# Performance work log

Hardware: AMD Instinct MI355X
Metric: run time of the kernel (lower is better)

Reference implementation:

```python
import jax, jax.numpy as jnp
import numpy as np

EPS = 1e-8
LAMBDA_SOFTMAX = 9.0
LAMBDA_LSE = 6.0
MARGIN = 0.2


def setup_inputs() -> dict:
    key = jax.random.key(0)
    k1, k2, k3 = jax.random.split(key, 3)
    B, R, W, D = 128, 36, 64, 1024
    im = jax.random.normal(k1, (B, R, D), dtype=jnp.float32)
    s = jax.random.normal(k2, (B, W, D), dtype=jnp.float32)
    s_l = jax.random.randint(k3, (B,), 8, W + 1, dtype=jnp.int32)
    return {"im": im, "s": s, "s_l": s_l}


def _xattn_scores_t2i(im, s, s_l):
    # im: [B, R, D] images; s: [B, W, D] captions; s_l: [B] caption lengths
    B, W = s.shape[0], s.shape[1]
    wmask = (jnp.arange(W)[None, :] < s_l[:, None]).astype(im.dtype)  # [B, W]

    def per_caption(args):
        cap, wm = args  # cap: [W, D], wm: [W]
        # raw attention: context=images, query=caption words -> [B, R, W]
        attn = jnp.einsum('ird,wd->irw', im, cap)
        # clipped_l2norm: leakyrelu(0.1) then l2norm over word dim; padded words zeroed
        attn = jax.nn.leaky_relu(attn, 0.1) * wm
        attn = attn / (jnp.sqrt(jnp.sum(attn * attn, axis=2, keepdims=True)) + EPS)
        # transpose to [B, W, R], softmax over regions with smoothing
        attn = jax.nn.softmax(jnp.swapaxes(attn, 1, 2) * LAMBDA_SOFTMAX, axis=2)
        # weighted image context per word: [B, W, D]
        wei = jnp.einsum('iwr,ird->iwd', attn, im)
        # cosine similarity between caption words and weighted context
        num = jnp.einsum('iwd,wd->iw', wei, cap)
        n_cap = jnp.sqrt(jnp.sum(cap * cap, axis=-1))      # [W]
        n_wei = jnp.sqrt(jnp.sum(wei * wei, axis=-1))      # [B, W]
        row = num / jnp.maximum(n_cap[None, :] * n_wei, EPS)
        # LogSumExp aggregation over valid words -> [B]
        return jnp.log(jnp.sum(jnp.exp(LAMBDA_LSE * row) * wm[None, :], axis=1)) / LAMBDA_LSE

    cols = jax.lax.map(per_caption, (s, wmask))  # [B_cap, B_img]
    return cols.T  # scores[i, j]: image i vs caption j


def reference(im, s, s_l):
    scores = _xattn_scores_t2i(im, s, s_l)  # [B, B]
    B = scores.shape[0]
    diag = jnp.diagonal(scores)[:, None]  # [B, 1]
    cost_s = jnp.clip(MARGIN + scores - diag, 0.0)       # caption retrieval
    cost_im = jnp.clip(MARGIN + scores - diag.T, 0.0)    # image retrieval
    off = 1.0 - jnp.eye(B, dtype=scores.dtype)
    cost_s = cost_s * off
    cost_im = cost_im * off
    # max_violation=True: hardest negatives
    cost_s = jnp.max(cost_s, axis=1)
    cost_im = jnp.max(cost_im, axis=0)
    return jnp.sum(cost_s) + jnp.sum(cost_im)
```

## Files before the change

### kernel.cpp

```cpp
#include <hip/hip_runtime.h>
#include <hip/hip_bf16.h>
#include <math.h>
#include <stdint.h>

#define NB 128
#define NR 36
#define NW 64
#define ND 1024
#define MT 48
#define EPSF 1e-8f
#define LAM_SM 9.0f
#define LAM_LSE 6.0f
#define MARGINF 0.2f

typedef _Float16 f16;
typedef f16 f16x4 __attribute__((ext_vector_type(4)));
typedef f16 f16x8 __attribute__((ext_vector_type(8)));
typedef float f32x4 __attribute__((ext_vector_type(4)));
typedef int i32x4 __attribute__((ext_vector_type(4)));
typedef int i32x8 __attribute__((ext_vector_type(8)));

__device__ __forceinline__ uint32_t pk_fp8x4(float4 v) {
    uint32_t w = 0;
    w = __builtin_amdgcn_cvt_pk_fp8_f32(v.x, v.y, w, false);
    w = __builtin_amdgcn_cvt_pk_fp8_f32(v.z, v.w, w, true);
    return w;
}


__global__ __launch_bounds__(256) void prep_kernel(
    const float* __restrict__ im, const float* __restrict__ s,
    uint8_t* __restrict__ im8, uint8_t* __restrict__ s8, float* __restrict__ ncap,
    f16* __restrict__ Mg16) {
    __shared__ __align__(16) char Gs[8192];
    const int b = blockIdx.x, y = blockIdx.y, t = threadIdx.x;

    if (y < 14) {
        const int lr = t >> 5, g = t & 31;
        const int row = y * 8 + lr;
        if (row < MT) {
            const int mi = row >> 4, l16 = row & 15;
            uint32_t* dstd = (uint32_t*)im8;
            if (row < NR) {
                const float4* src = (const float4*)(im + ((size_t)b * NR + row) * ND);
                #pragma unroll
                for (int e = 0; e < 8; ++e) {
                    int di = g + e * 32;
                    int kc = di >> 5, q = (di >> 3) & 3, bw = di & 7;
                    size_t dst = ((size_t)(b * 8 + kc) * 3 + mi) * 512
                                 + (q * 16 + l16) * 8 + bw;
                    dstd[dst] = pk_fp8x4(src[di]);
                }
            } else {
                #pragma unroll
                for (int e = 0; e < 8; ++e) {
                    int di = g + e * 32;
                    int kc = di >> 5, q = (di >> 3) & 3, bw = di & 7;
                    size_t dst = ((size_t)(b * 8 + kc) * 3 + mi) * 512
                                 + (q * 16 + l16) * 8 + bw;
                    dstd[dst] = 0u;
                }
            }
        } else {
            const int w = row - MT;
            const int nt = w >> 4, l16 = w & 15;
            const float4* src = (const float4*)(s + ((size_t)b * NW + w) * ND);
            uint32_t* dstd = (uint32_t*)s8;
            float ss = 0.f;
            #pragma unroll
            for (int e = 0; e < 8; ++e) {
                int di = g + e * 32;
                int kc = di >> 5, q = (di >> 3) & 3, bw = di & 7;
                float4 v = src[di];
                size_t dst = ((size_t)(b * 8 + kc) * 4 + nt) * 512
                             + (q * 16 + l16) * 8 + bw;
                dstd[dst] = pk_fp8x4(v);
                ss += v.x * v.x + v.y * v.y + v.z * v.z + v.w * v.w;
            }
            #pragma unroll
            for (int off = 1; off < 32; off <<= 1) ss += __shfl_xor(ss, off, 32);
            if (g == 0) ncap[b * NW + w] = sqrtf(ss);
        }
        return;
    }

    const int wave = t >> 6, lane = t & 63;
    const int quad = lane >> 4, l16 = lane & 15;
    const int nt = wave;
    f32x4 acc[3];
    acc[0] = (f32x4){0.f, 0.f, 0.f, 0.f};
    acc[1] = (f32x4){0.f, 0.f, 0.f, 0.f};
    acc[2] = (f32x4){0.f, 0.f, 0.f, 0.f};
    const float* imb = im + (size_t)b * NR * ND;

    for (int kk = 0; kk < ND; kk += 64) {
        for (int cidx = t; cidx < 512; cidx += 256) {
            int row = cidx >> 3, c = cidx & 7;
            f16x8 hv;
            if (row < NR) {
                const float4* sp = (const float4*)(imb + (size_t)row * ND + kk + c * 8);
                float4 v0 = sp[0], v1 = sp[1];
                hv = (f16x8){(f16)v0.x, (f16)v0.y, (f16)v0.z, (f16)v0.w,
                             (f16)v1.x, (f16)v1.y, (f16)v1.z, (f16)v1.w};
            } else {
                hv = (f16x8){(f16)0.f, (f16)0.f, (f16)0.f, (f16)0.f,
                             (f16)0.f, (f16)0.f, (f16)0.f, (f16)0.f};
            }
            *(f16x8*)(Gs + row * 128 + ((c ^ (row & 7)) * 16)) = hv;
        }
        __syncthreads();
        #pragma unroll
        for (int ks = 0; ks < 2; ++ks) {
            int brow = nt * 16 + l16;
            f16x8 bf = *(const f16x8*)(Gs + brow * 128 + (((ks * 4 + quad) ^ (brow & 7)) * 16));
            #pragma unroll
            for (int mt = 0; mt < 3; ++mt) {
                int arow = mt * 16 + l16;
                f16x8 af = *(const f16x8*)(Gs + arow * 128 + (((ks * 4 + quad) ^ (arow & 7)) * 16));
                acc[mt] = __builtin_amdgcn_mfma_f32_16x16x32_f16(af, bf, acc[mt], 0, 0, 0);
            }
        }
        __syncthreads();
    }
    f16* Mb = Mg16 + (size_t)b * (MT * NW);
    #pragma unroll
    for (int mt = 0; mt < 3; ++mt) {
        #pragma unroll
        for (int r = 0; r < 4; ++r) {
            int row = mt * 16 + quad * 4 + r;
            Mb[row * NW + nt * 16 + l16] = (f16)acc[mt][r];
        }
    }
}

__global__ __launch_bounds__(256) void fused_pair_kernel(
    const uint8_t* __restrict__ im8, const uint8_t* __restrict__ s8,
    const int* __restrict__ s_l, const f16* __restrict__ Mg16,
    const float* __restrict__ ncap, float* __restrict__ scores) {
    __shared__ __align__(16) char lds[32768];
    const int t = threadIdx.x;
    const int wave = t >> 6, lane = t & 63;
    const int quad = lane >> 4, l16 = lane & 15;
    const int wi = wave >> 1, wj = wave & 1;

    const int lin = blockIdx.x;
    const int gx = lin & 63, gy = lin >> 6;
    const int i = gy * 2 + wi;
    const int j = gx * 2 + wj;
    const int L = s_l[j];

    f32x4 acc[3][4];
    #pragma unroll
    for (int mi = 0; mi < 3; ++mi)
        #pragma unroll
        for (int nt = 0; nt < 4; ++nt)
            acc[mi][nt] = (f32x4){0.f, 0.f, 0.f, 0.f};

    const uint8_t* Afrag = im8 + (size_t)i * (8 * 3 * 2048) + lane * 32;
    const uint8_t* Bfrag = s8 + (size_t)j * (8 * 4 * 2048) + lane * 32;

    #pragma unroll 1
    for (int kc = 0; kc < 8; ++kc) {
        const uint8_t* Ak = Afrag + (size_t)kc * (3 * 2048);
        const uint8_t* Bk = Bfrag + (size_t)kc * (4 * 2048);
        i32x8 bf[4];
        #pragma unroll
        for (int nt = 0; nt < 4; ++nt)
            bf[nt] = *(const i32x8*)(Bk + nt * 2048);
        #pragma unroll
        for (int mi = 0; mi < 3; ++mi) {
            i32x8 af = *(const i32x8*)(Ak + mi * 2048);
            #pragma unroll
            for (int nt = 0; nt < 4; ++nt)
                acc[mi][nt] = __builtin_amdgcn_mfma_scale_f32_16x16x128_f8f6f4(
                    af, bf[nt], acc[mi][nt], 0, 0, 0, 0x7F, 0, 0x7F);
        }
    }

    char* waveE = lds + wave * 8192;
    {
        int col = lane;
        f16x8 z = {(f16)0.f,(f16)0.f,(f16)0.f,(f16)0.f,(f16)0.f,(f16)0.f,(f16)0.f,(f16)0.f};
        *(f16x8*)(waveE + col * 128 + ((6 ^ (col & 7)) * 16)) = z;
        *(f16x8*)(waveE + col * 128 + ((7 ^ (col & 7)) * 16)) = z;
    }

    float rn[3][4];
    #pragma unroll
    for (int mi = 0; mi < 3; ++mi) {
        #pragma unroll
        for (int r = 0; r < 4; ++r) {
            int row = mi * 16 + quad * 4 + r;
            float ss = 0.f;
            #pragma unroll
            for (int nt = 0; nt < 4; ++nt) {
                int col = nt * 16 + l16;
                float v = acc[mi][nt][r];
                float lv = v > 0.f ? v : 0.1f * v;
                if (col < L) ss += lv * lv;
            }
            ss += __shfl_xor(ss, 1, 64);
            ss += __shfl_xor(ss, 2, 64);
            ss += __shfl_xor(ss, 4, 64);
            ss += __shfl_xor(ss, 8, 64);
            rn[mi][r] = (row < NR) ? 1.0f / (sqrtf(ss) + EPSF) : 0.f;
        }
    }
    float cs[4] = {0.f, 0.f, 0.f, 0.f}, nu[4] = {0.f, 0.f, 0.f, 0.f};
    #pragma unroll
    for (int mi = 0; mi < 3; ++mi) {
        #pragma unroll
        for (int nt = 0; nt < 4; ++nt) {
            int col = nt * 16 + l16;
            f16x4 ew;
            #pragma unroll
            for (int r = 0; r < 4; ++r) {
                float v = acc[mi][nt][r];
                float lv = v > 0.f ? v : 0.1f * v;
                float e = __expf(LAM_SM * ((col < L) ? lv * rn[mi][r] : 0.f));
                ew[r] = (f16)e;
                if (mi * 16 + quad * 4 + r < NR) { cs[nt] += e; nu[nt] += e * v; }
            }
            int c = mi * 2 + (quad >> 1);
            *(f16x4*)(waveE + col * 128 + ((c ^ (col & 7)) * 16) + (quad & 1) * 8) = ew;
        }
    }
    #pragma unroll
    for (int nt = 0; nt < 4; ++nt) {
        cs[nt] += __shfl_xor(cs[nt], 16, 64); cs[nt] += __shfl_xor(cs[nt], 32, 64);
        nu[nt] += __shfl_xor(nu[nt], 16, 64); nu[nt] += __shfl_xor(nu[nt], 32, 64);
    }

    const f16* Mi = Mg16 + (size_t)i * (MT * NW);
    float qf[4] = {0.f, 0.f, 0.f, 0.f};
    #pragma unroll
    for (int mi = 0; mi < 3; ++mi) {
        f32x4 y[4];
        #pragma unroll
        for (int nt = 0; nt < 4; ++nt) y[nt] = (f32x4){0.f, 0.f, 0.f, 0.f};
        #pragma unroll
        for (int ks = 0; ks < 2; ++ks) {
            f16x8 aq = *(const f16x8*)(Mi + (mi * 16 + l16) * NW + ks * 32 + quad * 8);
            #pragma unroll
            for (int nt = 0; nt < 4; ++nt) {
                int col = nt * 16 + l16;
                int pch = (ks * 4 + quad) ^ (col & 7);
                f16x8 bq = *(const f16x8*)(waveE + col * 128 + pch * 16);
                y[nt] = __builtin_amdgcn_mfma_f32_16x16x32_f16(aq, bq, y[nt], 0, 0, 0);
            }
        }
        int row0 = mi * 16 + quad * 4;
        int c = row0 >> 3, sub = (row0 >> 2) & 1;
        #pragma unroll
        for (int nt = 0; nt < 4; ++nt) {
            int col = nt * 16 + l16;
            f16x4 ev = *(const f16x4*)(waveE + col * 128 + ((c ^ (col & 7)) * 16) + sub * 8);
            #pragma unroll
            for (int r = 0; r < 4; ++r) qf[nt] += y[nt][r] * (float)ev[r];
        }
    }
    #pragma unroll
    for (int nt = 0; nt < 4; ++nt) {
        qf[nt] += __shfl_xor(qf[nt], 16, 64); qf[nt] += __shfl_xor(qf[nt], 32, 64);
    }
    float lse = 0.f;
    #pragma unroll
    for (int nt = 0; nt < 4; ++nt) {
        int col = nt * 16 + l16;
        float num  = nu[nt] / cs[nt];
        float nwei = sqrtf(fmaxf(qf[nt], 0.f)) / cs[nt];
        float nc   = ncap[j * NW + col];
        float rowv = num / fmaxf(nc * nwei, EPSF);
        lse += (col < L) ? __expf(LAM_LSE * rowv) : 0.f;
    }
    lse += __shfl_xor(lse, 1, 64);
    lse += __shfl_xor(lse, 2, 64);
    lse += __shfl_xor(lse, 4, 64);
    lse += __shfl_xor(lse, 8, 64);
    if (lane == 0) scores[i * NB + j] = __logf(lse) / LAM_LSE;
}

__global__ __launch_bounds__(256) void loss_kernel(const float* __restrict__ S,
                                                   float* __restrict__ out) {
    __shared__ __align__(16) float Sl[NB * NB];
    __shared__ float part[NB];
    __shared__ float wsum[2];
    int t = threadIdx.x;
    for (int c = t; c < (NB * NB) / 4; c += 256)
        ((float4*)Sl)[c] = ((const float4*)S)[c];
    __syncthreads();
    if (t < NB) {
        float dii = Sl[t * NB + t];
        float rmax = 0.f, cmax = 0.f;
        for (int k = 0; k < NB; ++k) {
            if (k != t) {
                float vs = MARGINF + Sl[t * NB + k] - dii;
                rmax = fmaxf(rmax, fmaxf(vs, 0.f));
                float vi = MARGINF + Sl[k * NB + t] - dii;
                cmax = fmaxf(cmax, fmaxf(vi, 0.f));
            }
        }
        part[t] = rmax + cmax;
    }
    __syncthreads();
    if (t < NB) {
        float v = part[t];
        #pragma unroll
        for (int off = 1; off < 64; off <<= 1) v += __shfl_xor(v, off, 64);
        if ((t & 63) == 0) wsum[t >> 6] = v;
    }
    __syncthreads();
    if (t == 0) out[0] = wsum[0] + wsum[1];
}

extern "C" void kernel_launch(void* const* d_in, const int* in_sizes, int n_in,
                              void* d_out, int out_size, void* d_ws, size_t ws_size,
                              hipStream_t stream) {
    const float* im  = (const float*)d_in[0];
    const float* s   = (const float*)d_in[1];
    const int*   s_l = (const int*)d_in[2];

    float*   scores = (float*)d_ws;
    float*   ncap   = scores + NB * NB;
    f16*     Mg16   = (f16*)(ncap + NB * NW);
    uint8_t* im8    = (uint8_t*)(Mg16 + (size_t)NB * MT * NW);
    uint8_t* s8     = im8 + (size_t)NB * MT * ND;

    dim3 pgrid(NB, 15);
    prep_kernel<<<pgrid, 256, 0, stream>>>(im, s, im8, s8, ncap, Mg16);
    fused_pair_kernel<<<4096, 256, 0, stream>>>(im8, s8, s_l, Mg16, ncap, scores);
    loss_kernel<<<1, 256, 0, stream>>>(scores, (float*)d_out);
}
```

Measured before the change: 212.0 us.

## Double-buffer FP8 fragment loads in pair kernel and skew loss-kernel row reads

Replaces the rolled k-loop in the fused pair kernel with a fully unrolled, register double-buffered sequence. The global fragment loads for chunk k+1 are issued before the 12 MFMAs of chunk k, so memory latency overlaps with matrix compute. The loss kernel now walks each row starting at a per-thread rotated column, which spreads LDS accesses across banks instead of every thread hitting the same bank. The cost is roughly double the registers held for fragments, which may lower occupancy.

```diff
diff --git a/kernel.cpp b/kernel.cpp
--- a/kernel.cpp
+++ b/kernel.cpp
@@ -133,6 +133,38 @@
     }
 }
 
+
+__device__ __forceinline__ void load_frags(
+    const uint8_t* __restrict__ Af, const uint8_t* __restrict__ Bf, int kc,
+    i32x8& a0, i32x8& a1, i32x8& a2,
+    i32x8& b0, i32x8& b1, i32x8& b2, i32x8& b3) {
+    const uint8_t* Ak = Af + kc * (3 * 2048);
+    const uint8_t* Bk = Bf + kc * (4 * 2048);
+    a0 = *(const i32x8*)(Ak);
+    a1 = *(const i32x8*)(Ak + 2048);
+    a2 = *(const i32x8*)(Ak + 4096);
+    b0 = *(const i32x8*)(Bk);
+    b1 = *(const i32x8*)(Bk + 2048);
+    b2 = *(const i32x8*)(Bk + 4096);
+    b3 = *(const i32x8*)(Bk + 6144);
+}
+
+#define MFMA12(A0, A1, A2, B0, B1, B2, B3)                                        \
+    do {                                                                          \
+        acc[0][0] = __builtin_amdgcn_mfma_scale_f32_16x16x128_f8f6f4(A0, B0, acc[0][0], 0, 0, 0, 0x7F, 0, 0x7F); \
+        acc[0][1] = __builtin_amdgcn_mfma_scale_f32_16x16x128_f8f6f4(A0, B1, acc[0][1], 0, 0, 0, 0x7F, 0, 0x7F); \
+        acc[0][2] = __builtin_amdgcn_mfma_scale_f32_16x16x128_f8f6f4(A0, B2, acc[0][2], 0, 0, 0, 0x7F, 0, 0x7F); \
+        acc[0][3] = __builtin_amdgcn_mfma_scale_f32_16x16x128_f8f6f4(A0, B3, acc[0][3], 0, 0, 0, 0x7F, 0, 0x7F); \
+        acc[1][0] = __builtin_amdgcn_mfma_scale_f32_16x16x128_f8f6f4(A1, B0, acc[1][0], 0, 0, 0, 0x7F, 0, 0x7F); \
+        acc[1][1] = __builtin_amdgcn_mfma_scale_f32_16x16x128_f8f6f4(A1, B1, acc[1][1], 0, 0, 0, 0x7F, 0, 0x7F); \
+        acc[1][2] = __builtin_amdgcn_mfma_scale_f32_16x16x128_f8f6f4(A1, B2, acc[1][2], 0, 0, 0, 0x7F, 0, 0x7F); \
+        acc[1][3] = __builtin_amdgcn_mfma_scale_f32_16x16x128_f8f6f4(A1, B3, acc[1][3], 0, 0, 0, 0x7F, 0, 0x7F); \
+        acc[2][0] = __builtin_amdgcn_mfma_scale_f32_16x16x128_f8f6f4(A2, B0, acc[2][0], 0, 0, 0, 0x7F, 0, 0x7F); \
+        acc[2][1] = __builtin_amdgcn_mfma_scale_f32_16x16x128_f8f6f4(A2, B1, acc[2][1], 0, 0, 0, 0x7F, 0, 0x7F); \
+        acc[2][2] = __builtin_amdgcn_mfma_scale_f32_16x16x128_f8f6f4(A2, B2, acc[2][2], 0, 0, 0, 0x7F, 0, 0x7F); \
+        acc[2][3] = __builtin_amdgcn_mfma_scale_f32_16x16x128_f8f6f4(A2, B3, acc[2][3], 0, 0, 0, 0x7F, 0, 0x7F); \
+    } while (0)
+
 __global__ __launch_bounds__(256) void fused_pair_kernel(
     const uint8_t* __restrict__ im8, const uint8_t* __restrict__ s8,
     const int* __restrict__ s_l, const f16* __restrict__ Mg16,
@@ -159,23 +191,25 @@
     const uint8_t* Afrag = im8 + (size_t)i * (8 * 3 * 2048) + lane * 32;
     const uint8_t* Bfrag = s8 + (size_t)j * (8 * 4 * 2048) + lane * 32;
 
-    #pragma unroll 1
-    for (int kc = 0; kc < 8; ++kc) {
-        const uint8_t* Ak = Afrag + (size_t)kc * (3 * 2048);
-        const uint8_t* Bk = Bfrag + (size_t)kc * (4 * 2048);
-        i32x8 bf[4];
-        #pragma unroll
-        for (int nt = 0; nt < 4; ++nt)
-            bf[nt] = *(const i32x8*)(Bk + nt * 2048);
-        #pragma unroll
-        for (int mi = 0; mi < 3; ++mi) {
-            i32x8 af = *(const i32x8*)(Ak + mi * 2048);
-            #pragma unroll
-            for (int nt = 0; nt < 4; ++nt)
-                acc[mi][nt] = __builtin_amdgcn_mfma_scale_f32_16x16x128_f8f6f4(
-                    af, bf[nt], acc[mi][nt], 0, 0, 0, 0x7F, 0, 0x7F);
-        }
-    }
+    i32x8 xa0, xa1, xa2, xb0, xb1, xb2, xb3;
+    i32x8 ya0, ya1, ya2, yb0, yb1, yb2, yb3;
+
+    load_frags(Afrag, Bfrag, 0, xa0, xa1, xa2, xb0, xb1, xb2, xb3);
+    load_frags(Afrag, Bfrag, 1, ya0, ya1, ya2, yb0, yb1, yb2, yb3);
+    MFMA12(xa0, xa1, xa2, xb0, xb1, xb2, xb3);
+    load_frags(Afrag, Bfrag, 2, xa0, xa1, xa2, xb0, xb1, xb2, xb3);
+    MFMA12(ya0, ya1, ya2, yb0, yb1, yb2, yb3);
+    load_frags(Afrag, Bfrag, 3, ya0, ya1, ya2, yb0, yb1, yb2, yb3);
+    MFMA12(xa0, xa1, xa2, xb0, xb1, xb2, xb3);
+    load_frags(Afrag, Bfrag, 4, xa0, xa1, xa2, xb0, xb1, xb2, xb3);
+    MFMA12(ya0, ya1, ya2, yb0, yb1, yb2, yb3);
+    load_frags(Afrag, Bfrag, 5, ya0, ya1, ya2, yb0, yb1, yb2, yb3);
+    MFMA12(xa0, xa1, xa2, xb0, xb1, xb2, xb3);
+    load_frags(Afrag, Bfrag, 6, xa0, xa1, xa2, xb0, xb1, xb2, xb3);
+    MFMA12(ya0, ya1, ya2, yb0, yb1, yb2, yb3);
+    load_frags(Afrag, Bfrag, 7, ya0, ya1, ya2, yb0, yb1, yb2, yb3);
+    MFMA12(xa0, xa1, xa2, xb0, xb1, xb2, xb3);
+    MFMA12(ya0, ya1, ya2, yb0, yb1, yb2, yb3);
 
     char* waveE = lds + wave * 8192;
     {
@@ -293,9 +327,12 @@
         float dii = Sl[t * NB + t];
         float rmax = 0.f, cmax = 0.f;
         for (int k = 0; k < NB; ++k) {
+            int kk = (k + t) & (NB - 1);
+            if (kk != t) {
+                float vs = MARGINF + Sl[t * NB + kk] - dii;
+                rmax = fmaxf(rmax, fmaxf(vs, 0.f));
+            }
             if (k != t) {
-                float vs = MARGINF + Sl[t * NB + k] - dii;
-                rmax = fmaxf(rmax, fmaxf(vs, 0.f));
                 float vi = MARGINF + Sl[k * NB + t] - dii;
                 cmax = fmaxf(cmax, fmaxf(vi, 0.f));
             }
```

After: 221.1 us. 1.04x slower.
